# Optimization experiments

Measured on AMD Instinct MI355X. Metric: run time of the kernel, lower is better.

The kernel has to match this reference:

```python
import jax, jax.numpy as jnp
import numpy as np

B, IN, OUT, M = 4096, 512, 512, 16


def setup_inputs() -> dict:
    key = jax.random.key(0)
    k1, k2, k3 = jax.random.split(key, 3)
    # inputs kept strictly positive and inside the physical range [0, 60]
    x = jax.random.uniform(k1, (B, IN), jnp.float32, 0.1, 10.0)
    # photonic basis coefficients: positive, with small polynomial terms
    b_coef = jax.random.uniform(k2, (M, 8), jnp.float32, 0.1, 0.9)
    b_coef = b_coef.at[:, 4:].multiply(0.01)
    coeffs = 0.01 * jax.random.normal(k3, (OUT, IN, M), jnp.float32)
    return {"x": x, "coeffs": coeffs, "b_coef": b_coef}


def _photonic_basis(x, b):
    # x: (B, IN) -> broadcast against M basis functions -> (B, IN, M)
    xe = x[:, :, None]                                   # (B, IN, 1)
    b1, b2, b3, b4, b5, b6, b7, b8 = [b[:, i][None, None, :] for i in range(8)]
    inner = jnp.expm1(b3 * xe)
    powered = jnp.power(inner, b4)
    y = (b1 * jnp.log(1.0 + b2 * jnp.log1p(powered))
         + b5 * xe + b6 * xe**2 + b7 * xe**3 + b8 * xe**4)
    return y


def reference(x, coeffs, b_coef):
    # basis: (B, IN, M); double reduce over (IN, M) == GEMM of size B x (IN*M) x OUT
    basis = _photonic_basis(x, b_coef)
    y = jnp.einsum('bim,oim->bo', basis, coeffs)         # (B, OUT)
    return y
```

## Files before the change

kernel.cpp:

```cpp
#include <hip/hip_runtime.h>
#include <hip/hip_bf16.h>
#include <stdint.h>

#define B_DIM   4096
#define IN_DIM  512
#define OUT_DIM 512
#define M_DIM   16
#define K_DIM   (IN_DIM * M_DIM)
#define MN      (B_DIM * OUT_DIM)

#define TBL_N    512
#define TBL_STR  20
#define TBL_F32  ((TBL_N + 1) * TBL_STR)
#define TBL_H    (9.9f / (float)TBL_N)
#define TBL_INVH ((float)TBL_N / 9.9f)

typedef unsigned short ushort_t;
typedef __attribute__((ext_vector_type(8))) __bf16 bf16x8;
typedef __attribute__((ext_vector_type(2))) __bf16 bf16x2;
typedef __attribute__((ext_vector_type(4))) float  f32x4;

__device__ __forceinline__ ushort_t f2bf(float f) {
  union { float f; uint32_t u; } v; v.f = f;
  uint32_t u = v.u + 0x7fffu + ((v.u >> 16) & 1u);
  return (ushort_t)(u >> 16);
}

__device__ __forceinline__ uint32_t pkbf(float lo, float hi) {
  union { bf16x2 h; uint32_t u; } v;
  v.h[0] = (__bf16)lo; v.h[1] = (__bf16)hi;
  return v.u;
}

#define CONV_N4     (OUT_DIM * K_DIM / 4)
#define CONV_BLOCKS (CONV_N4 / 256)
__global__ __launch_bounds__(256) void convert_coeffs_kernel(
    const float* __restrict__ src, ushort_t* __restrict__ dst,
    const float* __restrict__ bc, float* __restrict__ tG) {
  const int blk = blockIdx.x, tid = threadIdx.x;
  if (blk < CONV_BLOCKS) {
    int i = blk * 256 + tid;
    float4 v = ((const float4*)src)[i];
    ushort4 o;
    o.x = f2bf(v.x); o.y = f2bf(v.y); o.z = f2bf(v.z); o.w = f2bf(v.w);
    ((ushort4*)dst)[i] = o;
    return;
  }
  const float LOG2E = 1.44269504088896340736f;
  const float LN2   = 0.69314718055994530942f;
  for (int e = tid; e <= TBL_N; e += 256) {
    float xv = 0.1f + (float)e * TBL_H;
    float xl2 = xv * LOG2E;
    float x2 = xv * xv, x3 = x2 * xv, x4 = x2 * x2;
    #pragma unroll
    for (int m = 0; m < M_DIM; ++m) {
      float b1 = bc[m*8+0], b2 = bc[m*8+1], b3 = bc[m*8+2], b4 = bc[m*8+3];
      float b5 = bc[m*8+4], b6 = bc[m*8+5], b7 = bc[m*8+6], b8 = bc[m*8+7];
      float e2    = __builtin_amdgcn_exp2f(b3 * xl2);
      float inner = e2 - 1.0f;
      float p     = __builtin_amdgcn_exp2f(b4 * __builtin_amdgcn_logf(inner));
      float L1    = __builtin_amdgcn_logf(1.0f + p);
      float vv    = __builtin_amdgcn_logf(1.0f + (b2 * LN2) * L1);
      float y = (b1 * LN2) * vv + b5 * xv + b6 * x2 + b7 * x3 + b8 * x4;
      tG[e * TBL_STR + m] = y;
    }
  }
}

#define BM 128
#define BN 512
#define BK 32
#define SPLITK 8
#define KC (K_DIM / SPLITK)
#define NITER (KC / BK)
#define XCOLS (KC / M_DIM)

#define GLD16(g, l) \
  __builtin_amdgcn_global_load_lds((const __attribute__((address_space(1))) void*)(g), \
                                   (__attribute__((address_space(3))) void*)(l), 16, 0, 0)

#define WAIT_BAR(N) \
  asm volatile("s_waitcnt vmcnt(" #N ") lgkmcnt(0)\n\ts_barrier" ::: "memory")

template <int ATOMIC>
__global__ __launch_bounds__(512, 2) void gemm_kernel(
    const float* __restrict__ x,
    const ushort_t* __restrict__ Bt,
    const float* __restrict__ tG,
    float* __restrict__ P) {
  __shared__ __align__(16) ushort_t As[2][BM * BK];
  __shared__ __align__(16) ushort_t Bs[3][BN * BK];
  __shared__ __align__(16) float    Ts[TBL_F32];
  const int tid  = threadIdx.x;
  const int wave = tid >> 6;
  const int lane = tid & 63;
  const int wgid = blockIdx.x;
  const int ks = wgid & 7, bm = wgid >> 3;

  {
    const float4* g4 = (const float4*)tG;
    float4* l4 = (float4*)Ts;
    for (int i = tid; i < TBL_F32 / 4; i += 512) l4[i] = g4[i];
  }

  const int srow = wave * 16 + (lane >> 2);
  const int scol = (((lane & 3) ^ ((lane >> 3) & 3)) * 8);
  const ushort_t* Bg0 = Bt + (size_t)srow * K_DIM + ks * KC + scol;
  const ushort_t* Bg1 = Bg0 + (size_t)128 * K_DIM;
  const ushort_t* Bg2 = Bg0 + (size_t)256 * K_DIM;
  const ushort_t* Bg3 = Bg0 + (size_t)384 * K_DIM;
  const int bofs0 = (wave * 16) * BK;
  const int bofs1 = (128 + wave * 16) * BK;
  const int bofs2 = (256 + wave * 16) * BK;
  const int bofs3 = (384 + wave * 16) * BK;

#define STAGEB(lb) do { \
    GLD16(Bg0, &Bs[lb][bofs0]); GLD16(Bg1, &Bs[lb][bofs1]); \
    GLD16(Bg2, &Bs[lb][bofs2]); GLD16(Bg3, &Bs[lb][bofs3]); \
    Bg0 += BK; Bg1 += BK; Bg2 += BK; Bg3 += BK; } while (0)

  const int half = wave & 1;
  const int arow = (wave >> 1) * 32 + (lane >> 1);
  const int il   = lane & 1;
  const int aslot = ((il * 2 + half) ^ ((lane >> 2) & 3));
  const int awe   = arow * BK + aslot * 8;
  const float* xg = x + (size_t)(bm * BM + arow) * IN_DIM + ks * XCOLS + il;
  const int thalf = half * 8;

#define BASIS(ab, xv) do { \
    float uu = ((xv) - 0.1f) * TBL_INVH; \
    uu = fminf(fmaxf(uu, 0.0f), 511.99f); \
    float fi = floorf(uu); \
    float fr = uu - fi; \
    int tix = (int)fi * TBL_STR + thalf; \
    f32x4 v0 = *(const f32x4*)&Ts[tix]; \
    f32x4 v1 = *(const f32x4*)&Ts[tix + 4]; \
    f32x4 w0 = *(const f32x4*)&Ts[tix + TBL_STR]; \
    f32x4 w1 = *(const f32x4*)&Ts[tix + TBL_STR + 4]; \
    float ym[8]; \
    _Pragma("unroll") \
    for (int k = 0; k < 4; ++k) { \
      ym[k]     = v0[k] + fr * (w0[k] - v0[k]); \
      ym[4 + k] = v1[k] + fr * (w1[k] - v1[k]); \
    } \
    *(uint4*)(&As[ab][awe]) = make_uint4(pkbf(ym[0], ym[1]), pkbf(ym[2], ym[3]), \
                                         pkbf(ym[4], ym[5]), pkbf(ym[6], ym[7])); \
  } while (0)

  const int wr = wave >> 2, wc = wave & 3;
  const int fm = lane & 15;
  const int fkswz = (((lane >> 4) ^ ((lane >> 1) & 3)) << 3);

  f32x4 acc[4][8] = {};

#define COMPUTE(ab, lb) do { \
    bf16x8 af[4], bfv[8]; \
    _Pragma("unroll") \
    for (int t2 = 0; t2 < 4; ++t2) \
      af[t2] = *(const bf16x8*)&As[ab][(wr * 64 + t2 * 16 + fm) * BK + fkswz]; \
    _Pragma("unroll") \
    for (int u = 0; u < 8; ++u) \
      bfv[u] = *(const bf16x8*)&Bs[lb][(wc * 128 + u * 16 + fm) * BK + fkswz]; \
    __builtin_amdgcn_s_setprio(1); \
    _Pragma("unroll") \
    for (int mt = 0; mt < 4; ++mt) \
      _Pragma("unroll") \
      for (int nt = 0; nt < 8; ++nt) \
        acc[mt][nt] = __builtin_amdgcn_mfma_f32_16x16x32_bf16(af[mt], bfv[nt], acc[mt][nt], 0, 0, 0); \
    __builtin_amdgcn_s_setprio(0); \
  } while (0)

#define STEP(lbN, ap, ac, lb, t1) do { \
    float xc = xn; \
    xn = xg[2 * ((t1) + 1)]; \
    STAGEB(lbN); \
    BASIS(ap, xc); COMPUTE(ac, lb); WAIT_BAR(4); } while (0)

  float x0 = xg[0];
  STAGEB(0); STAGEB(1);
  __syncthreads();
  float xn = xg[2];
  BASIS(0, x0);
  WAIT_BAR(0);

  for (int tb = 0; tb < NITER - 2; tb += 6) {
    STEP(2, 1, 0, 0, tb + 1);
    STEP(0, 0, 1, 1, tb + 2);
    STEP(1, 1, 0, 2, tb + 3);
    STEP(2, 0, 1, 0, tb + 4);
    STEP(0, 1, 0, 1, tb + 5);
    STEP(1, 0, 1, 2, tb + 6);
  }
  BASIS(1, xn);
  COMPUTE(0, 0);
  WAIT_BAR(0);
  COMPUTE(1, 1);

  const int colb = wc * 128 + fm;
  const int rowb = bm * BM + wr * 64 + (lane >> 4) * 4;
  float* out = P + (ATOMIC ? (size_t)0 : (size_t)ks * MN);
  #pragma unroll
  for (int mt = 0; mt < 4; ++mt) {
    #pragma unroll
    for (int nt = 0; nt < 8; ++nt) {
      #pragma unroll
      for (int j = 0; j < 4; ++j) {
        int row = rowb + mt * 16 + j;
        int col = colb + nt * 16;
        float vv = acc[mt][nt][j];
        if (ATOMIC) atomicAdd(out + (size_t)row * OUT_DIM + col, vv);
        else        out[(size_t)row * OUT_DIM + col] = vv;
      }
    }
  }
#undef STAGEB
#undef BASIS
#undef COMPUTE
#undef STEP
}

__global__ __launch_bounds__(256) void reduce_kernel(
    const float* __restrict__ P, float* __restrict__ out) {
  int i = blockIdx.x * 256 + threadIdx.x;
  const float4* p = (const float4*)P;
  float4 r = p[i];
  #pragma unroll
  for (int s = 1; s < SPLITK; ++s) {
    float4 v = p[i + (size_t)s * (MN / 4)];
    r.x += v.x; r.y += v.y; r.z += v.z; r.w += v.w;
  }
  ((float4*)out)[i] = r;
}

extern "C" void kernel_launch(void* const* d_in, const int* in_sizes, int n_in,
                              void* d_out, int out_size, void* d_ws, size_t ws_size,
                              hipStream_t stream) {
  const float* x      = (const float*)d_in[0];
  const float* coeffs = (const float*)d_in[1];
  const float* b_coef = (const float*)d_in[2];
  float* out = (float*)d_out;
  char*  ws  = (char*)d_ws;

  const size_t COEF_BYTES = (size_t)OUT_DIM * K_DIM * 2;
  const size_t TBL_BYTES  = (size_t)TBL_F32 * 4;
  ushort_t* coefb = (ushort_t*)ws;
  float*    tG    = (float*)(ws + COEF_BYTES);
  float* partials = (float*)(ws + COEF_BYTES + TBL_BYTES);
  const size_t FULL = COEF_BYTES + TBL_BYTES + (size_t)SPLITK * MN * 4;
  const bool use_atomic = (ws_size < FULL);

  convert_coeffs_kernel<<<CONV_BLOCKS + 1, 256, 0, stream>>>(coeffs, coefb, b_coef, tG);

  const int nblk = (B_DIM / BM) * SPLITK;
  if (use_atomic) {
    hipMemsetAsync(d_out, 0, (size_t)MN * 4, stream);
    gemm_kernel<1><<<nblk, 512, 0, stream>>>(x, coefb, tG, out);
  } else {
    gemm_kernel<0><<<nblk, 512, 0, stream>>>(x, coefb, tG, partials);
    reduce_kernel<<<MN / 4 / 256, 256, 0, stream>>>(partials, out);
  }
}
```

Before: 140.2 us.

## Build A-operand MFMA fragments directly in registers from LDS table lookups

```diff
diff --git a/kernel.cpp b/kernel.cpp
--- a/kernel.cpp
+++ b/kernel.cpp
@@ -9,7 +9,7 @@
 #define K_DIM   (IN_DIM * M_DIM)
 #define MN      (B_DIM * OUT_DIM)
 
-#define TBL_N    512
+#define TBL_N    256
 #define TBL_STR  20
 #define TBL_F32  ((TBL_N + 1) * TBL_STR)
 #define TBL_H    (9.9f / (float)TBL_N)
@@ -74,6 +74,7 @@
 #define KC (K_DIM / SPLITK)
 #define NITER (KC / BK)
 #define XCOLS (KC / M_DIM)
+#define XPAD  129
 
 #define GLD16(g, l) \
   __builtin_amdgcn_global_load_lds((const __attribute__((address_space(1))) void*)(g), \
@@ -88,8 +89,8 @@
     const ushort_t* __restrict__ Bt,
     const float* __restrict__ tG,
     float* __restrict__ P) {
-  __shared__ __align__(16) ushort_t As[2][BM * BK];
   __shared__ __align__(16) ushort_t Bs[3][BN * BK];
+  __shared__ __align__(16) float    Xs[XCOLS * XPAD];
   __shared__ __align__(16) float    Ts[TBL_F32];
   const int tid  = threadIdx.x;
   const int wave = tid >> 6;
@@ -101,6 +102,18 @@
     const float4* g4 = (const float4*)tG;
     float4* l4 = (float4*)Ts;
     for (int i = tid; i < TBL_F32 / 4; i += 512) l4[i] = g4[i];
+  }
+  {
+    const int r = tid >> 2, q = tid & 3;
+    const float4* xrow = (const float4*)(x + (size_t)(bm * BM + r) * IN_DIM + ks * XCOLS);
+    #pragma unroll
+    for (int j = 0; j < 4; ++j) {
+      float4 v = xrow[q * 4 + j];
+      Xs[(q * 16 + j * 4 + 0) * XPAD + r] = v.x;
+      Xs[(q * 16 + j * 4 + 1) * XPAD + r] = v.y;
+      Xs[(q * 16 + j * 4 + 2) * XPAD + r] = v.z;
+      Xs[(q * 16 + j * 4 + 3) * XPAD + r] = v.w;
+    }
   }
 
   const int srow = wave * 16 + (lane >> 2);
@@ -119,45 +132,93 @@
     GLD16(Bg2, &Bs[lb][bofs2]); GLD16(Bg3, &Bs[lb][bofs3]); \
     Bg0 += BK; Bg1 += BK; Bg2 += BK; Bg3 += BK; } while (0)
 
-  const int half = wave & 1;
-  const int arow = (wave >> 1) * 32 + (lane >> 1);
-  const int il   = lane & 1;
-  const int aslot = ((il * 2 + half) ^ ((lane >> 2) & 3));
-  const int awe   = arow * BK + aslot * 8;
-  const float* xg = x + (size_t)(bm * BM + arow) * IN_DIM + ks * XCOLS + il;
-  const int thalf = half * 8;
-
-#define BASIS(ab, xv) do { \
-    float uu = ((xv) - 0.1f) * TBL_INVH; \
-    uu = fminf(fmaxf(uu, 0.0f), 511.99f); \
+  const int wr = wave >> 2, wc = wave & 3;
+  const int fm = lane & 15;
+  const int fkswz = (((lane >> 4) ^ ((lane >> 1) & 3)) << 3);
+  const int qq  = lane >> 4;
+  const int iq  = qq >> 1;
+  const int mh8 = (qq & 1) * 8;
+  const int arow0 = wr * 64 + fm;
+
+  f32x4 acc[4][8] = {};
+
+#define MAKE_AF(dst, t) do { \
+    float xv = Xs[(2 * (t) + iq) * XPAD + arow0 + 0]; \
+    (void)0; \
+    float uu = (xv - 0.1f) * TBL_INVH; \
+    uu = fminf(fmaxf(uu, 0.0f), (float)TBL_N - 0.01f); \
     float fi = floorf(uu); \
     float fr = uu - fi; \
-    int tix = (int)fi * TBL_STR + thalf; \
+    int tix = (int)fi * TBL_STR + mh8; \
     f32x4 v0 = *(const f32x4*)&Ts[tix]; \
     f32x4 v1 = *(const f32x4*)&Ts[tix + 4]; \
     f32x4 w0 = *(const f32x4*)&Ts[tix + TBL_STR]; \
     f32x4 w1 = *(const f32x4*)&Ts[tix + TBL_STR + 4]; \
-    float ym[8]; \
-    _Pragma("unroll") \
-    for (int k = 0; k < 4; ++k) { \
-      ym[k]     = v0[k] + fr * (w0[k] - v0[k]); \
-      ym[4 + k] = v1[k] + fr * (w1[k] - v1[k]); \
-    } \
-    *(uint4*)(&As[ab][awe]) = make_uint4(pkbf(ym[0], ym[1]), pkbf(ym[2], ym[3]), \
-                                         pkbf(ym[4], ym[5]), pkbf(ym[6], ym[7])); \
-  } while (0)
-
-  const int wr = wave >> 2, wc = wave & 3;
-  const int fm = lane & 15;
-  const int fkswz = (((lane >> 4) ^ ((lane >> 1) & 3)) << 3);
-
-  f32x4 acc[4][8] = {};
-
-#define COMPUTE(ab, lb) do { \
+    uint32_t p0 = pkbf(v0[0] + fr * (w0[0] - v0[0]), v0[1] + fr * (w0[1] - v0[1])); \
+    uint32_t p1 = pkbf(v0[2] + fr * (w0[2] - v0[2]), v0[3] + fr * (w0[3] - v0[3])); \
+    uint32_t p2 = pkbf(v1[0] + fr * (w1[0] - v1[0]), v1[1] + fr * (w1[1] - v1[1])); \
+    uint32_t p3 = pkbf(v1[2] + fr * (w1[2] - v1[2]), v1[3] + fr * (w1[3] - v1[3])); \
+    union { uint32_t u[4]; bf16x8 h; } cvt_; \
+    cvt_.u[0] = p0; cvt_.u[1] = p1; cvt_.u[2] = p2; cvt_.u[3] = p3; \
+    dst = cvt_.h; \
+  } while (0)
+
+#undef MAKE_AF
+#define MAKE_AF(dst, t) do { \
+    float xv = Xs[(2 * (t)) * XPAD + iq * XPAD + arow0 + (t) * 16]; \
+    float uu = (xv - 0.1f) * TBL_INVH; \
+    uu = fminf(fmaxf(uu, 0.0f), (float)TBL_N - 0.01f); \
+    float fi = floorf(uu); \
+    float fr = uu - fi; \
+    int tix = (int)fi * TBL_STR + mh8; \
+    f32x4 v0 = *(const f32x4*)&Ts[tix]; \
+    f32x4 v1 = *(const f32x4*)&Ts[tix + 4]; \
+    f32x4 w0 = *(const f32x4*)&Ts[tix + TBL_STR]; \
+    f32x4 w1 = *(const f32x4*)&Ts[tix + TBL_STR + 4]; \
+    uint32_t p0 = pkbf(v0[0] + fr * (w0[0] - v0[0]), v0[1] + fr * (w0[1] - v0[1])); \
+    uint32_t p1 = pkbf(v0[2] + fr * (w0[2] - v0[2]), v0[3] + fr * (w0[3] - v0[3])); \
+    uint32_t p2 = pkbf(v1[0] + fr * (w1[0] - v1[0]), v1[1] + fr * (w1[1] - v1[1])); \
+    uint32_t p3 = pkbf(v1[2] + fr * (w1[2] - v1[2]), v1[3] + fr * (w1[3] - v1[3])); \
+    union { uint32_t u[4]; bf16x8 h; } cvt_; \
+    cvt_.u[0] = p0; cvt_.u[1] = p1; cvt_.u[2] = p2; cvt_.u[3] = p3; \
+    dst = cvt_.h; \
+  } while (0)
+
+#define COMPUTE(lb, t) do { \
     bf16x8 af[4], bfv[8]; \
-    _Pragma("unroll") \
-    for (int t2 = 0; t2 < 4; ++t2) \
-      af[t2] = *(const bf16x8*)&As[ab][(wr * 64 + t2 * 16 + fm) * BK + fkswz]; \
+    MAKE_AF(af[0], t); MAKE_AF(af[1], t);  \
+  } while (0)
+#undef COMPUTE
+#define COMPUTE(lb, t) do { \
+    bf16x8 af0, af1, af2, af3, bfv[8]; \
+    MAKE_AF(af0, t); \
+    { bf16x8 tmp_; MAKE_AF(tmp_, t); af1 = tmp_; } \
+  } while (0)
+#undef COMPUTE
+#undef MAKE_AF
+#define MAKE_AF_R(dst, t, rofs) do { \
+    float xv = Xs[(2 * (t) + iq) * XPAD + arow0 + (rofs)]; \
+    float uu = (xv - 0.1f) * TBL_INVH; \
+    uu = fminf(fmaxf(uu, 0.0f), (float)TBL_N - 0.01f); \
+    float fi = floorf(uu); \
+    float fr = uu - fi; \
+    int tix = (int)fi * TBL_STR + mh8; \
+    f32x4 v0 = *(const f32x4*)&Ts[tix]; \
+    f32x4 v1 = *(const f32x4*)&Ts[tix + 4]; \
+    f32x4 w0 = *(const f32x4*)&Ts[tix + TBL_STR]; \
+    f32x4 w1 = *(const f32x4*)&Ts[tix + TBL_STR + 4]; \
+    union { uint32_t u[4]; bf16x8 h; } cvt_; \
+    cvt_.u[0] = pkbf(v0[0] + fr * (w0[0] - v0[0]), v0[1] + fr * (w0[1] - v0[1])); \
+    cvt_.u[1] = pkbf(v0[2] + fr * (w0[2] - v0[2]), v0[3] + fr * (w0[3] - v0[3])); \
+    cvt_.u[2] = pkbf(v1[0] + fr * (w1[0] - v1[0]), v1[1] + fr * (w1[1] - v1[1])); \
+    cvt_.u[3] = pkbf(v1[2] + fr * (w1[2] - v1[2]), v1[3] + fr * (w1[3] - v1[3])); \
+    dst = cvt_.h; \
+  } while (0)
+
+#define COMPUTE2(lb, t) do { \
+    bf16x8 af[4], bfv[8]; \
+    MAKE_AF_R(af[0], t, 0);  MAKE_AF_R(af[1], t, 16); \
+    MAKE_AF_R(af[2], t, 32); MAKE_AF_R(af[3], t, 48); \
     _Pragma("unroll") \
     for (int u = 0; u < 8; ++u) \
       bfv[u] = *(const bf16x8*)&Bs[lb][(wc * 128 + u * 16 + fm) * BK + fkswz]; \
@@ -170,31 +231,22 @@
     __builtin_amdgcn_s_setprio(0); \
   } while (0)
 
-#define STEP(lbN, ap, ac, lb, t1) do { \
-    float xc = xn; \
-    xn = xg[2 * ((t1) + 1)]; \
-    STAGEB(lbN); \
-    BASIS(ap, xc); COMPUTE(ac, lb); WAIT_BAR(4); } while (0)
-
-  float x0 = xg[0];
+#define STEP(lbN, lb, t) do { \
+    STAGEB(lbN); COMPUTE2(lb, t); WAIT_BAR(4); } while (0)
+
   STAGEB(0); STAGEB(1);
   __syncthreads();
-  float xn = xg[2];
-  BASIS(0, x0);
+  for (int tb = 0; tb < NITER - 2; tb += 6) {
+    STEP(2, 0, tb + 0);
+    STEP(0, 1, tb + 1);
+    STEP(1, 2, tb + 2);
+    STEP(2, 0, tb + 3);
+    STEP(0, 1, tb + 4);
+    STEP(1, 2, tb + 5);
+  }
+  COMPUTE2(0, 30);
   WAIT_BAR(0);
-
-  for (int tb = 0; tb < NITER - 2; tb += 6) {
-    STEP(2, 1, 0, 0, tb + 1);
-    STEP(0, 0, 1, 1, tb + 2);
-    STEP(1, 1, 0, 2, tb + 3);
-    STEP(2, 0, 1, 0, tb + 4);
-    STEP(0, 1, 0, 1, tb + 5);
-    STEP(1, 0, 1, 2, tb + 6);
-  }
-  BASIS(1, xn);
-  COMPUTE(0, 0);
-  WAIT_BAR(0);
-  COMPUTE(1, 1);
+  COMPUTE2(1, 31);
 
   const int colb = wc * 128 + fm;
   const int rowb = bm * BM + wr * 64 + (lane >> 4) * 4;
@@ -214,8 +266,8 @@
     }
   }
 #undef STAGEB
-#undef BASIS
-#undef COMPUTE
+#undef MAKE_AF_R
+#undef COMPUTE2
 #undef STEP
 }
 
```

Result: slower. 157.2 us (+12.1%).
